# Kernel tuning notes

Measured on AMD Instinct MI355X. Metric: run time of the kernel, lower is better.

The kernel has to match this reference:

```python
import jax, jax.numpy as jnp
import numpy as np

H, W, C = 56, 56, 192
WS, SS = 7, 3          # window_size, shift_size
NH, HD = 6, 32         # num_heads, head_dim
N = WS * WS            # tokens per window = 49
HIDDEN = 4 * C
EPS = 1e-5


def _rel_pos_index():
    coords = np.stack(np.meshgrid(np.arange(WS), np.arange(WS), indexing='ij'))  # (2,ws,ws)
    flat = coords.reshape(2, -1)
    rel = flat[:, :, None] - flat[:, None, :]            # (2,N,N)
    rel = rel.transpose(1, 2, 0)
    rel[:, :, 0] += WS - 1
    rel[:, :, 1] += WS - 1
    rel[:, :, 0] *= 2 * WS - 1
    return rel.sum(-1)                                   # (N,N) int


def _attn_mask():
    img = np.zeros((H, W))
    cnt = 0
    for hs in (slice(0, -WS), slice(-WS, -SS), slice(-SS, None)):
        for ws_ in (slice(0, -WS), slice(-WS, -SS), slice(-SS, None)):
            img[hs, ws_] = cnt
            cnt += 1
    mw = img.reshape(H // WS, WS, W // WS, WS).transpose(0, 2, 1, 3).reshape(-1, N)  # (nW,N)
    diff = mw[:, None, :] - mw[:, :, None]
    return np.where(diff != 0, -100.0, 0.0).astype(np.float32)  # (nW,N,N)


REL_IDX = jnp.asarray(_rel_pos_index())
ATTN_MASK = jnp.asarray(_attn_mask())


def _ln(x, w, b):
    mu = x.mean(-1, keepdims=True)
    var = ((x - mu) ** 2).mean(-1, keepdims=True)
    return (x - mu) * jax.lax.rsqrt(var + EPS) * w + b


def _window_partition(x):
    # (B,H,W,C) -> (B*nW, N, C)
    B = x.shape[0]
    x = x.reshape(B, H // WS, WS, W // WS, WS, C)
    x = x.transpose(0, 1, 3, 2, 4, 5)
    return x.reshape(-1, N, C)


def _window_reverse(win, B):
    # (B*nW, N, C) -> (B,H,W,C)
    x = win.reshape(B, H // WS, W // WS, WS, WS, C)
    x = x.transpose(0, 1, 3, 2, 4, 5)
    return x.reshape(B, H, W, C)


def setup_inputs() -> dict:
    key = jax.random.key(0)
    ks = jax.random.split(key, 16)
    s = 0.02
    return {
        'x': jax.random.normal(ks[0], (64, H * W, C), jnp.float32),
        'norm1_w': jnp.ones((C,), jnp.float32),
        'norm1_b': jnp.zeros((C,), jnp.float32),
        'qkv_w': jax.random.normal(ks[1], (C, 3 * C), jnp.float32) * s,
        'qkv_b': jnp.zeros((3 * C,), jnp.float32),
        'rpb': jax.random.normal(ks[2], ((2 * WS - 1) ** 2, NH), jnp.float32) * s,
        'proj_w': jax.random.normal(ks[3], (C, C), jnp.float32) * s,
        'proj_b': jnp.zeros((C,), jnp.float32),
        'norm2_w': jnp.ones((C,), jnp.float32),
        'norm2_b': jnp.zeros((C,), jnp.float32),
        'fc1_w': jax.random.normal(ks[4], (C, HIDDEN), jnp.float32) * s,
        'fc1_b': jnp.zeros((HIDDEN,), jnp.float32),
        'fc2_w': jax.random.normal(ks[5], (HIDDEN, C), jnp.float32) * s,
        'fc2_b': jnp.zeros((C,), jnp.float32),
    }


def reference(x, norm1_w, norm1_b, qkv_w, qkv_b, rpb, proj_w, proj_b,
              norm2_w, norm2_b, fc1_w, fc1_b, fc2_w, fc2_b):
    B = x.shape[0]
    nW = (H // WS) * (W // WS)
    shortcut = x
    h = _ln(x, norm1_w, norm1_b).reshape(B, H, W, C)
    # cyclic shift
    h = jnp.roll(h, shift=(-SS, -SS), axis=(1, 2))
    xw = _window_partition(h)                                   # (B*nW, N, C)
    # windowed MHA
    qkv = (xw @ qkv_w + qkv_b).reshape(-1, N, 3, NH, HD).transpose(2, 0, 3, 1, 4)
    q, k, v = qkv[0], qkv[1], qkv[2]                            # (Bn, NH, N, HD)
    scale = HD ** -0.5
    attn = jnp.einsum('bhnd,bhmd->bhnm', q * scale, k)          # (Bn, NH, N, N)
    bias = rpb[REL_IDX.reshape(-1)].reshape(N, N, NH).transpose(2, 0, 1)
    attn = attn + bias[None]
    attn = attn.reshape(B, nW, NH, N, N) + ATTN_MASK[None, :, None]
    attn = jax.nn.softmax(attn.reshape(-1, NH, N, N), axis=-1)
    out = jnp.einsum('bhnm,bhmd->bhnd', attn, v)
    out = out.transpose(0, 2, 1, 3).reshape(-1, N, C)
    out = out @ proj_w + proj_b
    # reverse windows + un-shift
    h = _window_reverse(out, B)
    h = jnp.roll(h, shift=(SS, SS), axis=(1, 2)).reshape(B, H * W, C)
    x = shortcut + h
    # MLP (exact GELU, as torch nn.GELU default)
    m = _ln(x, norm2_w, norm2_b)
    m = jax.nn.gelu(m @ fc1_w + fc1_b, approximate=False)
    m = m @ fc2_w + fc2_b
    return x + m
```

## Files before the change

### kernel.cpp

```cpp
#include <hip/hip_runtime.h>
#include <hip/hip_bf16.h>

typedef __hip_bfloat16 bf16;
typedef __attribute__((ext_vector_type(8))) short short8;
typedef __attribute__((ext_vector_type(4))) short short4v;
typedef __attribute__((ext_vector_type(4))) float floatx4;

__device__ __forceinline__ floatx4 mfma16(short8 a, short8 b, floatx4 c) {
  return __builtin_amdgcn_mfma_f32_16x16x32_bf16(a, b, c, 0, 0, 0);
}

__device__ __forceinline__ float wave_sum(float v) {
#pragma unroll
  for (int off = 1; off < 64; off <<= 1) v += __shfl_xor(v, off);
  return v;
}

__device__ __forceinline__ short8 lds_frag(const char* base, int row, int kb) {
  return *(const short8*)(base + row * 384 + (kb ^ ((row & 7) << 4)));
}
__device__ __forceinline__ short8 lds_frag128(const char* base, int row, int kb) {
  return *(const short8*)(base + row * 128 + (kb ^ ((row & 7) << 4)));
}

__global__ __launch_bounds__(256) void k_wt(const float* __restrict__ w,
                                            bf16* __restrict__ wt, int K, int N) {
  int id = blockIdx.x * 256 + threadIdx.x;
  if (id < K * N) {
    int n = id / K;
    int k = id - n * K;
    wt[id] = __float2bfloat16(w[(long)k * N + n]);
  }
}

template <bool GATHER>
__global__ __launch_bounds__(256) void k_ln(const float* __restrict__ xin,
                                            const float* __restrict__ w,
                                            const float* __restrict__ b,
                                            bf16* __restrict__ out) {
  const int lane = threadIdx.x & 63;
  const long row = (long)blockIdx.x * 4 + (threadIdx.x >> 6);
  long srow;
  if (GATHER) {
    int win = (int)(row / 49);
    int token = (int)(row - (long)win * 49);
    int bimg = win >> 6, wi = (win & 63) >> 3, wj = win & 7;
    int ti = token / 7, tj = token - ti * 7;
    int h = wi * 7 + ti + 3; if (h >= 56) h -= 56;
    int ww = wj * 7 + tj + 3; if (ww >= 56) ww -= 56;
    srow = (long)bimg * 3136 + h * 56 + ww;
  } else {
    srow = row;
  }
  const float* src = xin + srow * 192;
  float v0 = src[lane], v1 = src[lane + 64], v2 = src[lane + 128];
  float mu = wave_sum(v0 + v1 + v2) * (1.f / 192.f);
  float d0 = v0 - mu, d1 = v1 - mu, d2 = v2 - mu;
  float var = wave_sum(d0 * d0 + d1 * d1 + d2 * d2) * (1.f / 192.f);
  float rs = rsqrtf(var + 1e-5f);
  bf16* dst = out + row * 192;
  dst[lane]       = __float2bfloat16(d0 * rs * w[lane] + b[lane]);
  dst[lane + 64]  = __float2bfloat16(d1 * rs * w[lane + 64] + b[lane + 64]);
  dst[lane + 128] = __float2bfloat16(d2 * rs * w[lane + 128] + b[lane + 128]);
}

__global__ __launch_bounds__(384, 1) void k_swin(const bf16* __restrict__ xw,
                                                 const bf16* __restrict__ wq,
                                                 const float* __restrict__ qkvb,
                                                 const float* __restrict__ rpb,
                                                 const bf16* __restrict__ wp,
                                                 const float* __restrict__ projb,
                                                 const float* __restrict__ xres,
                                                 float* __restrict__ outf) {
  __shared__ __align__(16) char As[64 * 384];
  __shared__ __align__(16) bf16 QKP[6][5120];
  __shared__ __align__(16) bf16 Vts[6][32 * 72];
  const int t = threadIdx.x, lane = t & 63, wid = t >> 6;
  const int lanelo = lane & 15, quad = lane >> 4;
  const int w = blockIdx.x;
  const long rowbase = (long)w * 49;
  bf16* Qs = QKP[wid];
  bf16* Ks = Qs + 2560;
  bf16* Ps = Qs;
  bf16* Vt = Vts[wid];

  {
    const char* src = (const char*)(xw + rowbase * 192);
#pragma unroll
    for (int i = 0; i < 4; i++) {
      int c = i * 384 + t;
      int r = c / 24, j = c - r * 24;
      uint4 v;
      if (r < 49) v = *(const uint4*)(src + (long)r * 384 + j * 16);
      else { v.x = 0u; v.y = 0u; v.z = 0u; v.w = 0u; }
      *(uint4*)(As + r * 384 + ((j * 16) ^ ((r & 7) << 4))) = v;
    }
  }

  const int w_in = w & 63, wiw = w_in >> 3, wjw = w_in & 7;
  int cTi[4], cTj[4], cLab[4];
  bool cval[4];
#pragma unroll
  for (int ni = 0; ni < 4; ni++) {
    int j = ni * 16 + lanelo;
    cval[ni] = (j < 49);
    if (j > 48) j = 48;
    int ti = j / 7, tj = j - ti * 7;
    int rr = wiw * 7 + ti, cc = wjw * 7 + tj;
    cTi[ni] = ti; cTj[ni] = tj;
    cLab[ni] = ((rr < 49) ? 0 : (rr < 53 ? 1 : 2)) * 3 +
               ((cc < 49) ? 0 : (cc < 53 ? 1 : 2));
  }
  __syncthreads();

  const float scale = 0.17677669529663687f;

  {
    floatx4 aq[4][6];
#pragma unroll
    for (int mi = 0; mi < 4; mi++)
#pragma unroll
      for (int ni = 0; ni < 6; ni++) aq[mi][ni] = (floatx4){0.f, 0.f, 0.f, 0.f};
#pragma unroll
    for (int kk = 0; kk < 6; kk++) {
      const int kb = kk * 64 + quad * 16;
      short8 af[4];
#pragma unroll
      for (int mi = 0; mi < 4; mi++) af[mi] = lds_frag(As, mi * 16 + lanelo, kb);
#pragma unroll
      for (int ni = 0; ni < 6; ni++) {
        const int wrow = (ni >> 1) * 192 + wid * 32 + (ni & 1) * 16 + lanelo;
        short8 bf = *(const short8*)((const char*)wq + (long)wrow * 384 + kb);
#pragma unroll
        for (int mi = 0; mi < 4; mi++) aq[mi][ni] = mfma16(af[mi], bf, aq[mi][ni]);
      }
    }
#pragma unroll
    for (int ni = 0; ni < 6; ni++) {
      const int p = ni >> 1;
      const int d = (ni & 1) * 16 + lanelo;
      const float bb = qkvb[p * 192 + wid * 32 + d];
      if (p < 2) {
        bf16* dst = (p == 0) ? Qs : Ks;
#pragma unroll
        for (int mi = 0; mi < 4; mi++)
#pragma unroll
          for (int reg = 0; reg < 4; reg++) {
            int tok = mi * 16 + quad * 4 + reg;
            dst[tok * 40 + d] = __float2bfloat16(aq[mi][ni][reg] + bb);
          }
      } else {
#pragma unroll
        for (int mi = 0; mi < 4; mi++) {
          union { short4v s; bf16 hh[4]; } pv;
#pragma unroll
          for (int reg = 0; reg < 4; reg++)
            pv.hh[reg] = __float2bfloat16(aq[mi][ni][reg] + bb);
          *(short4v*)(&Vt[d * 72 + mi * 16 + quad * 4]) = pv.s;
        }
      }
    }
  }

  float rinv[16];
  {
    floatx4 aS[4][4];
#pragma unroll
    for (int mi = 0; mi < 4; mi++) {
      short8 aqf = *(const short8*)(&Qs[(mi * 16 + lanelo) * 40 + quad * 8]);
#pragma unroll
      for (int ni = 0; ni < 4; ni++) {
        short8 bk = *(const short8*)(&Ks[(ni * 16 + lanelo) * 40 + quad * 8]);
        aS[mi][ni] = mfma16(aqf, bk, (floatx4){0.f, 0.f, 0.f, 0.f});
      }
    }
#pragma unroll
    for (int mi = 0; mi < 4; mi++) {
#pragma unroll
      for (int reg = 0; reg < 4; reg++) {
        int i = mi * 16 + quad * 4 + reg;
        if (i > 48) i = 48;
        int ti = i / 7, tj = i - ti * 7;
        int rr = wiw * 7 + ti, cc = wjw * 7 + tj;
        int rlab = ((rr < 49) ? 0 : (rr < 53 ? 1 : 2)) * 3 +
                   ((cc < 49) ? 0 : (cc < 53 ? 1 : 2));
        float sv[4];
        float mx = -1e30f;
#pragma unroll
        for (int ni = 0; ni < 4; ni++) {
          float s;
          if (cval[ni]) {
            int ridx = (ti - cTi[ni] + 6) * 13 + (tj - cTj[ni] + 6);
            float bb = rpb[ridx * 6 + wid];
            if (rlab != cLab[ni]) bb -= 100.f;
            s = aS[mi][ni][reg] * scale + bb;
          } else {
            s = -1e30f;
          }
          sv[ni] = s;
          mx = fmaxf(mx, s);
        }
        mx = fmaxf(mx, __shfl_xor(mx, 1));
        mx = fmaxf(mx, __shfl_xor(mx, 2));
        mx = fmaxf(mx, __shfl_xor(mx, 4));
        mx = fmaxf(mx, __shfl_xor(mx, 8));
        float sum = 0.f;
#pragma unroll
        for (int ni = 0; ni < 4; ni++) {
          float p = __expf(sv[ni] - mx);
          sv[ni] = p;
          sum += p;
        }
        sum += __shfl_xor(sum, 1);
        sum += __shfl_xor(sum, 2);
        sum += __shfl_xor(sum, 4);
        sum += __shfl_xor(sum, 8);
        rinv[mi * 4 + reg] = 1.f / sum;
#pragma unroll
        for (int ni = 0; ni < 4; ni++) aS[mi][ni][reg] = sv[ni];
      }
    }
#pragma unroll
    for (int mi = 0; mi < 4; mi++)
#pragma unroll
      for (int ni = 0; ni < 4; ni++)
#pragma unroll
        for (int reg = 0; reg < 4; reg++)
          Ps[(mi * 16 + quad * 4 + reg) * 72 + ni * 16 + lanelo] =
              __float2bfloat16(aS[mi][ni][reg]);
  }

  floatx4 aO[4][2];
#pragma unroll
  for (int mi = 0; mi < 4; mi++)
#pragma unroll
    for (int ni = 0; ni < 2; ni++) aO[mi][ni] = (floatx4){0.f, 0.f, 0.f, 0.f};
#pragma unroll
  for (int ks = 0; ks < 2; ks++) {
#pragma unroll
    for (int mi = 0; mi < 4; mi++) {
      short8 ap = *(const short8*)(&Ps[(mi * 16 + lanelo) * 72 + ks * 32 + quad * 8]);
#pragma unroll
      for (int ni = 0; ni < 2; ni++) {
        short8 bv = *(const short8*)(&Vt[(ni * 16 + lanelo) * 72 + ks * 32 + quad * 8]);
        aO[mi][ni] = mfma16(ap, bv, aO[mi][ni]);
      }
    }
  }
  __syncthreads();

#pragma unroll
  for (int mi = 0; mi < 4; mi++)
#pragma unroll
    for (int ni = 0; ni < 2; ni++)
#pragma unroll
      for (int reg = 0; reg < 4; reg++) {
        int tok = mi * 16 + quad * 4 + reg;
        int cb = 2 * (wid * 32 + ni * 16 + lanelo);
        *(bf16*)(As + tok * 384 + (cb ^ ((tok & 7) << 4))) =
            __float2bfloat16(aO[mi][ni][reg] * rinv[mi * 4 + reg]);
      }
  __syncthreads();

  floatx4 accp[4][2];
#pragma unroll
  for (int mi = 0; mi < 4; mi++)
#pragma unroll
    for (int ni = 0; ni < 2; ni++) accp[mi][ni] = (floatx4){0.f, 0.f, 0.f, 0.f};
#pragma unroll
  for (int kk = 0; kk < 6; kk++) {
    const int kb = kk * 64 + quad * 16;
    short8 af[4];
#pragma unroll
    for (int mi = 0; mi < 4; mi++) af[mi] = lds_frag(As, mi * 16 + lanelo, kb);
#pragma unroll
    for (int ni = 0; ni < 2; ni++) {
      const int wrow = wid * 32 + ni * 16 + lanelo;
      short8 bf = *(const short8*)((const char*)wp + (long)wrow * 384 + kb);
#pragma unroll
      for (int mi = 0; mi < 4; mi++) accp[mi][ni] = mfma16(af[mi], bf, accp[mi][ni]);
    }
  }
#pragma unroll
  for (int mi = 0; mi < 4; mi++)
#pragma unroll
    for (int reg = 0; reg < 4; reg++) {
      const int tok = mi * 16 + quad * 4 + reg;
      if (tok < 49) {
        int ti = tok / 7, tj = tok - ti * 7;
        int hh = wiw * 7 + ti + 3; if (hh >= 56) hh -= 56;
        int ww2 = wjw * 7 + tj + 3; if (ww2 >= 56) ww2 -= 56;
        const long orow = (long)(w >> 6) * 3136 + hh * 56 + ww2;
#pragma unroll
        for (int ni = 0; ni < 2; ni++) {
          const int c = wid * 32 + ni * 16 + lanelo;
          outf[orow * 192 + c] = accp[mi][ni][reg] + projb[c] + xres[orow * 192 + c];
        }
      }
    }
}

__global__ __launch_bounds__(256, 4) void k_mlp(float* xres,
                                                const float* __restrict__ lw,
                                                const float* __restrict__ lb,
                                                const bf16* __restrict__ w1t,
                                                const float* __restrict__ b1,
                                                const bf16* __restrict__ w2t,
                                                const float* __restrict__ b2) {
  __shared__ __align__(16) char As[64 * 384];
  __shared__ __align__(16) char Hs[2][64 * 128];
  const int t = threadIdx.x, lane = t & 63, wid = t >> 6;
  const int lanelo = lane & 15, quad = lane >> 4;
  const long row0 = (long)blockIdx.x * 64;

  for (int i = 0; i < 16; i++) {
    int r = wid * 16 + i;
    const float* src = xres + (row0 + r) * 192;
    float v0 = src[lane], v1 = src[lane + 64], v2 = src[lane + 128];
    float mu = wave_sum(v0 + v1 + v2) * (1.f / 192.f);
    float d0 = v0 - mu, d1 = v1 - mu, d2 = v2 - mu;
    float var = wave_sum(d0 * d0 + d1 * d1 + d2 * d2) * (1.f / 192.f);
    float rs = rsqrtf(var + 1e-5f);
    int sw = (r & 7) << 4;
    *(bf16*)(As + r * 384 + ((2 * lane) ^ sw)) =
        __float2bfloat16(d0 * rs * lw[lane] + lb[lane]);
    *(bf16*)(As + r * 384 + ((128 + 2 * lane) ^ sw)) =
        __float2bfloat16(d1 * rs * lw[lane + 64] + lb[lane + 64]);
    *(bf16*)(As + r * 384 + ((256 + 2 * lane) ^ sw)) =
        __float2bfloat16(d2 * rs * lw[lane + 128] + lb[lane + 128]);
  }

  floatx4 acc2[4][3];
#pragma unroll
  for (int mi = 0; mi < 4; mi++)
#pragma unroll
    for (int ni = 0; ni < 3; ni++) acc2[mi][ni] = (floatx4){0.f, 0.f, 0.f, 0.f};

  __syncthreads();

  const int hcol = wid * 16 + lanelo;
  const int ocol0 = wid * 48;

  for (int nc = 0; nc < 12; nc++) {
    const char* w1p = (const char*)w1t + (long)(nc * 64 + hcol) * 384;
    floatx4 acc1[4];
#pragma unroll
    for (int mi = 0; mi < 4; mi++) acc1[mi] = (floatx4){0.f, 0.f, 0.f, 0.f};
#pragma unroll
    for (int kk = 0; kk < 6; kk++) {
      const int kb = kk * 64 + quad * 16;
      short8 bf = *(const short8*)(w1p + kb);
#pragma unroll
      for (int mi = 0; mi < 4; mi++) {
        short8 af = lds_frag(As, mi * 16 + lanelo, kb);
        acc1[mi] = mfma16(af, bf, acc1[mi]);
      }
    }

    char* H = Hs[nc & 1];
    const float b1v = b1[nc * 64 + hcol];
#pragma unroll
    for (int mi = 0; mi < 4; mi++)
#pragma unroll
      for (int reg = 0; reg < 4; reg++) {
        int r = mi * 16 + quad * 4 + reg;
        float v = acc1[mi][reg] + b1v;
        v = 0.5f * v * (1.f + erff(v * 0.70710678118654752f));
        *(bf16*)(H + r * 128 + ((2 * hcol) ^ ((r & 7) << 4))) =
            __float2bfloat16(v);
      }
    __syncthreads();

#pragma unroll
    for (int ks = 0; ks < 2; ks++) {
      const int kb = ks * 64 + quad * 16;
      short8 ha[4];
#pragma unroll
      for (int mi = 0; mi < 4; mi++)
        ha[mi] = lds_frag128(H, mi * 16 + lanelo, kb);
#pragma unroll
      for (int ni = 0; ni < 3; ni++) {
        short8 bv = *(const short8*)((const char*)w2t +
                                     (long)(ocol0 + ni * 16 + lanelo) * 1536 +
                                     nc * 128 + kb);
#pragma unroll
        for (int mi = 0; mi < 4; mi++)
          acc2[mi][ni] = mfma16(ha[mi], bv, acc2[mi][ni]);
      }
    }
  }

#pragma unroll
  for (int mi = 0; mi < 4; mi++)
#pragma unroll
    for (int ni = 0; ni < 3; ni++) {
      const int c = ocol0 + ni * 16 + lanelo;
      const float b2v = b2[c];
#pragma unroll
      for (int reg = 0; reg < 4; reg++) {
        const long g = (row0 + mi * 16 + quad * 4 + reg) * 192 + c;
        xres[g] = acc2[mi][ni][reg] + b2v + xres[g];
      }
    }
}

extern "C" void kernel_launch(void* const* d_in, const int* in_sizes, int n_in,
                              void* d_out, int out_size, void* d_ws, size_t ws_size,
                              hipStream_t stream) {
  const float* x     = (const float*)d_in[0];
  const float* n1w   = (const float*)d_in[1];
  const float* n1b   = (const float*)d_in[2];
  const float* qkvw  = (const float*)d_in[3];
  const float* qkvb  = (const float*)d_in[4];
  const float* rpb   = (const float*)d_in[5];
  const float* projw = (const float*)d_in[6];
  const float* projb = (const float*)d_in[7];
  const float* n2w   = (const float*)d_in[8];
  const float* n2b   = (const float*)d_in[9];
  const float* fc1w  = (const float*)d_in[10];
  const float* fc1b  = (const float*)d_in[11];
  const float* fc2w  = (const float*)d_in[12];
  const float* fc2b  = (const float*)d_in[13];
  float* outf = (float*)d_out;

  char* ws = (char*)d_ws;
  bf16* xw      = (bf16*)(ws + 0);
  bf16* wt_qkv  = (bf16*)(ws + 154140672LL);
  bf16* wt_proj = (bf16*)(ws + 154140672LL + 221184LL);
  bf16* wt_fc1  = (bf16*)(ws + 154140672LL + 294912LL);
  bf16* wt_fc2  = (bf16*)(ws + 154140672LL + 589824LL);

  k_wt<<<dim3((192 * 576 + 255) / 256), 256, 0, stream>>>(qkvw, wt_qkv, 192, 576);
  k_wt<<<dim3((192 * 192 + 255) / 256), 256, 0, stream>>>(projw, wt_proj, 192, 192);
  k_wt<<<dim3((192 * 768 + 255) / 256), 256, 0, stream>>>(fc1w, wt_fc1, 192, 768);
  k_wt<<<dim3((768 * 192 + 255) / 256), 256, 0, stream>>>(fc2w, wt_fc2, 768, 192);

  k_ln<true><<<dim3(50176), 256, 0, stream>>>(x, n1w, n1b, xw);

  k_swin<<<dim3(4096), 384, 0, stream>>>(xw, wt_qkv, qkvb, rpb, wt_proj, projb,
                                         x, outf);

  k_mlp<<<dim3(3136), 256, 0, stream>>>(outf, n2w, n2b, wt_fc1, fc1b,
                                        wt_fc2, fc2b);
}
```

Measured before the change: 995.6 us.

## Split each attention head across two waves in swin kernel with 768 threads

The windowed attention kernel now runs 12 waves per block instead of 6. Each head is handled by two waves that each own 32 query rows, and the proj GEMM is split into 16-column slices per wave. This cuts per-wave register pressure and serial work, with launch bounds raised to allow multiple blocks per CU. The cost is extra block-wide barriers, since each half-head's Q/K/V must be visible to its partner wave, and duplicated weight-fragment loads in the QKV GEMM.

Result: slower. 1.063 ms (+6.8%).

```diff
diff --git a/kernel.cpp b/kernel.cpp
--- a/kernel.cpp
+++ b/kernel.cpp
@@ -64,7 +64,7 @@
   dst[lane + 128] = __float2bfloat16(d2 * rs * w[lane + 128] + b[lane + 128]);
 }
 
-__global__ __launch_bounds__(384, 1) void k_swin(const bf16* __restrict__ xw,
+__global__ __launch_bounds__(768, 3) void k_swin(const bf16* __restrict__ xw,
                                                  const bf16* __restrict__ wq,
                                                  const float* __restrict__ qkvb,
                                                  const float* __restrict__ rpb,
@@ -73,22 +73,23 @@
                                                  const float* __restrict__ xres,
                                                  float* __restrict__ outf) {
   __shared__ __align__(16) char As[64 * 384];
-  __shared__ __align__(16) bf16 QKP[6][5120];
-  __shared__ __align__(16) bf16 Vts[6][32 * 72];
+  __shared__ __align__(16) bf16 HeadMem[6][7424];
   const int t = threadIdx.x, lane = t & 63, wid = t >> 6;
+  const int head = wid >> 1, half = wid & 1;
   const int lanelo = lane & 15, quad = lane >> 4;
   const int w = blockIdx.x;
   const long rowbase = (long)w * 49;
-  bf16* Qs = QKP[wid];
+  const int r0 = half * 32;
+  bf16* Qs = HeadMem[head];
   bf16* Ks = Qs + 2560;
+  bf16* Vt = Qs + 5120;
   bf16* Ps = Qs;
-  bf16* Vt = Vts[wid];
 
   {
     const char* src = (const char*)(xw + rowbase * 192);
 #pragma unroll
-    for (int i = 0; i < 4; i++) {
-      int c = i * 384 + t;
+    for (int i = 0; i < 2; i++) {
+      int c = i * 768 + t;
       int r = c / 24, j = c - r * 24;
       uint4 v;
       if (r < 49) v = *(const uint4*)(src + (long)r * 384 + j * 16);
@@ -116,58 +117,60 @@
   const float scale = 0.17677669529663687f;
 
   {
-    floatx4 aq[4][6];
-#pragma unroll
-    for (int mi = 0; mi < 4; mi++)
+    floatx4 aq[2][6];
+#pragma unroll
+    for (int mi = 0; mi < 2; mi++)
 #pragma unroll
       for (int ni = 0; ni < 6; ni++) aq[mi][ni] = (floatx4){0.f, 0.f, 0.f, 0.f};
 #pragma unroll
     for (int kk = 0; kk < 6; kk++) {
       const int kb = kk * 64 + quad * 16;
-      short8 af[4];
-#pragma unroll
-      for (int mi = 0; mi < 4; mi++) af[mi] = lds_frag(As, mi * 16 + lanelo, kb);
+      short8 af[2];
+#pragma unroll
+      for (int mi = 0; mi < 2; mi++)
+        af[mi] = lds_frag(As, r0 + mi * 16 + lanelo, kb);
 #pragma unroll
       for (int ni = 0; ni < 6; ni++) {
-        const int wrow = (ni >> 1) * 192 + wid * 32 + (ni & 1) * 16 + lanelo;
+        const int wrow = (ni >> 1) * 192 + head * 32 + (ni & 1) * 16 + lanelo;
         short8 bf = *(const short8*)((const char*)wq + (long)wrow * 384 + kb);
 #pragma unroll
-        for (int mi = 0; mi < 4; mi++) aq[mi][ni] = mfma16(af[mi], bf, aq[mi][ni]);
+        for (int mi = 0; mi < 2; mi++) aq[mi][ni] = mfma16(af[mi], bf, aq[mi][ni]);
       }
     }
 #pragma unroll
     for (int ni = 0; ni < 6; ni++) {
       const int p = ni >> 1;
       const int d = (ni & 1) * 16 + lanelo;
-      const float bb = qkvb[p * 192 + wid * 32 + d];
+      const float bb = qkvb[p * 192 + head * 32 + d];
       if (p < 2) {
         bf16* dst = (p == 0) ? Qs : Ks;
 #pragma unroll
-        for (int mi = 0; mi < 4; mi++)
+        for (int mi = 0; mi < 2; mi++)
 #pragma unroll
           for (int reg = 0; reg < 4; reg++) {
-            int tok = mi * 16 + quad * 4 + reg;
+            int tok = r0 + mi * 16 + quad * 4 + reg;
             dst[tok * 40 + d] = __float2bfloat16(aq[mi][ni][reg] + bb);
           }
       } else {
 #pragma unroll
-        for (int mi = 0; mi < 4; mi++) {
+        for (int mi = 0; mi < 2; mi++) {
           union { short4v s; bf16 hh[4]; } pv;
 #pragma unroll
           for (int reg = 0; reg < 4; reg++)
             pv.hh[reg] = __float2bfloat16(aq[mi][ni][reg] + bb);
-          *(short4v*)(&Vt[d * 72 + mi * 16 + quad * 4]) = pv.s;
+          *(short4v*)(&Vt[d * 72 + r0 + mi * 16 + quad * 4]) = pv.s;
         }
       }
     }
   }
-
-  float rinv[16];
+  __syncthreads();
+
+  float rinv[8];
+  floatx4 aS[2][4];
   {
-    floatx4 aS[4][4];
-#pragma unroll
-    for (int mi = 0; mi < 4; mi++) {
-      short8 aqf = *(const short8*)(&Qs[(mi * 16 + lanelo) * 40 + quad * 8]);
+#pragma unroll
+    for (int mi = 0; mi < 2; mi++) {
+      short8 aqf = *(const short8*)(&Qs[(r0 + mi * 16 + lanelo) * 40 + quad * 8]);
 #pragma unroll
       for (int ni = 0; ni < 4; ni++) {
         short8 bk = *(const short8*)(&Ks[(ni * 16 + lanelo) * 40 + quad * 8]);
@@ -175,10 +178,10 @@
       }
     }
 #pragma unroll
-    for (int mi = 0; mi < 4; mi++) {
+    for (int mi = 0; mi < 2; mi++) {
 #pragma unroll
       for (int reg = 0; reg < 4; reg++) {
-        int i = mi * 16 + quad * 4 + reg;
+        int i = r0 + mi * 16 + quad * 4 + reg;
         if (i > 48) i = 48;
         int ti = i / 7, tj = i - ti * 7;
         int rr = wiw * 7 + ti, cc = wjw * 7 + tj;
@@ -191,7 +194,7 @@
           float s;
           if (cval[ni]) {
             int ridx = (ti - cTi[ni] + 6) * 13 + (tj - cTj[ni] + 6);
-            float bb = rpb[ridx * 6 + wid];
+            float bb = rpb[ridx * 6 + head];
             if (rlab != cLab[ni]) bb -= 100.f;
             s = aS[mi][ni][reg] * scale + bb;
           } else {
@@ -220,26 +223,28 @@
         for (int ni = 0; ni < 4; ni++) aS[mi][ni][reg] = sv[ni];
       }
     }
-#pragma unroll
-    for (int mi = 0; mi < 4; mi++)
-#pragma unroll
-      for (int ni = 0; ni < 4; ni++)
-#pragma unroll
-        for (int reg = 0; reg < 4; reg++)
-          Ps[(mi * 16 + quad * 4 + reg) * 72 + ni * 16 + lanelo] =
-              __float2bfloat16(aS[mi][ni][reg]);
-  }
-
-  floatx4 aO[4][2];
-#pragma unroll
-  for (int mi = 0; mi < 4; mi++)
+  }
+  __syncthreads();
+
+#pragma unroll
+  for (int mi = 0; mi < 2; mi++)
+#pragma unroll
+    for (int ni = 0; ni < 4; ni++)
+#pragma unroll
+      for (int reg = 0; reg < 4; reg++)
+        Ps[(r0 + mi * 16 + quad * 4 + reg) * 72 + ni * 16 + lanelo] =
+            __float2bfloat16(aS[mi][ni][reg]);
+
+  floatx4 aO[2][2];
+#pragma unroll
+  for (int mi = 0; mi < 2; mi++)
 #pragma unroll
     for (int ni = 0; ni < 2; ni++) aO[mi][ni] = (floatx4){0.f, 0.f, 0.f, 0.f};
 #pragma unroll
   for (int ks = 0; ks < 2; ks++) {
 #pragma unroll
-    for (int mi = 0; mi < 4; mi++) {
-      short8 ap = *(const short8*)(&Ps[(mi * 16 + lanelo) * 72 + ks * 32 + quad * 8]);
+    for (int mi = 0; mi < 2; mi++) {
+      short8 ap = *(const short8*)(&Ps[(r0 + mi * 16 + lanelo) * 72 + ks * 32 + quad * 8]);
 #pragma unroll
       for (int ni = 0; ni < 2; ni++) {
         short8 bv = *(const short8*)(&Vt[(ni * 16 + lanelo) * 72 + ks * 32 + quad * 8]);
@@ -247,38 +252,32 @@
       }
     }
   }
-  __syncthreads();
-
-#pragma unroll
-  for (int mi = 0; mi < 4; mi++)
+
+#pragma unroll
+  for (int mi = 0; mi < 2; mi++)
 #pragma unroll
     for (int ni = 0; ni < 2; ni++)
 #pragma unroll
       for (int reg = 0; reg < 4; reg++) {
-        int tok = mi * 16 + quad * 4 + reg;
-        int cb = 2 * (wid * 32 + ni * 16 + lanelo);
+        int tok = r0 + mi * 16 + quad * 4 + reg;
+        int cb = 2 * (head * 32 + ni * 16 + lanelo);
         *(bf16*)(As + tok * 384 + (cb ^ ((tok & 7) << 4))) =
             __float2bfloat16(aO[mi][ni][reg] * rinv[mi * 4 + reg]);
       }
   __syncthreads();
 
-  floatx4 accp[4][2];
-#pragma unroll
-  for (int mi = 0; mi < 4; mi++)
-#pragma unroll
-    for (int ni = 0; ni < 2; ni++) accp[mi][ni] = (floatx4){0.f, 0.f, 0.f, 0.f};
+  floatx4 accp[4];
+#pragma unroll
+  for (int mi = 0; mi < 4; mi++) accp[mi] = (floatx4){0.f, 0.f, 0.f, 0.f};
 #pragma unroll
   for (int kk = 0; kk < 6; kk++) {
     const int kb = kk * 64 + quad * 16;
-    short8 af[4];
-#pragma unroll
-    for (int mi = 0; mi < 4; mi++) af[mi] = lds_frag(As, mi * 16 + lanelo, kb);
-#pragma unroll
-    for (int ni = 0; ni < 2; ni++) {
-      const int wrow = wid * 32 + ni * 16 + lanelo;
-      short8 bf = *(const short8*)((const char*)wp + (long)wrow * 384 + kb);
-#pragma unroll
-      for (int mi = 0; mi < 4; mi++) accp[mi][ni] = mfma16(af[mi], bf, accp[mi][ni]);
+    short8 bf = *(const short8*)((const char*)wp +
+                                 (long)(wid * 16 + lanelo) * 384 + kb);
+#pragma unroll
+    for (int mi = 0; mi < 4; mi++) {
+      short8 af = lds_frag(As, mi * 16 + lanelo, kb);
+      accp[mi] = mfma16(af, bf, accp[mi]);
     }
   }
 #pragma unroll
@@ -291,11 +290,8 @@
         int hh = wiw * 7 + ti + 3; if (hh >= 56) hh -= 56;
         int ww2 = wjw * 7 + tj + 3; if (ww2 >= 56) ww2 -= 56;
         const long orow = (long)(w >> 6) * 3136 + hh * 56 + ww2;
-#pragma unroll
-        for (int ni = 0; ni < 2; ni++) {
-          const int c = wid * 32 + ni * 16 + lanelo;
-          outf[orow * 192 + c] = accp[mi][ni][reg] + projb[c] + xres[orow * 192 + c];
-        }
+        const int c = wid * 16 + lanelo;
+        outf[orow * 192 + c] = accp[mi][reg] + projb[c] + xres[orow * 192 + c];
       }
     }
 }
@@ -437,7 +433,7 @@
 
   k_ln<true><<<dim3(50176), 256, 0, stream>>>(x, n1w, n1b, xw);
 
-  k_swin<<<dim3(4096), 384, 0, stream>>>(xw, wt_qkv, qkvb, rpb, wt_proj, projb,
+  k_swin<<<dim3(4096), 768, 0, stream>>>(xw, wt_qkv, qkvb, rpb, wt_proj, projb,
                                          x, outf);
 
   k_mlp<<<dim3(3136), 256, 0, stream>>>(outf, n2w, n2b, wt_fc1, fc1b,
```
